# Kernel optimization log

Measured on AMD Instinct MI355X. Metric: run time of the kernel, lower is better.

## Reference

```python
import jax, jax.numpy as jnp
import numpy as np

B, S, D = 2, 2048, 2048
H, KVH, DH = 16, 4, 128  # n_heads, n_kv_heads, head_dim
N_REP = H // KVH
THETA = 10000.0


def setup_inputs() -> dict:
    key = jax.random.key(0)
    ks = jax.random.split(key, 6)
    x = jax.random.normal(ks[0], (B, S, D), dtype=jnp.float32)
    wq = jax.random.normal(ks[1], (H * DH, D), dtype=jnp.float32) * (D ** -0.5)
    wk = jax.random.normal(ks[2], (KVH * DH, D), dtype=jnp.float32) * (D ** -0.5)
    wv = jax.random.normal(ks[3], (KVH * DH, D), dtype=jnp.float32) * (D ** -0.5)
    wo = jax.random.normal(ks[4], (D, H * DH), dtype=jnp.float32) * (D ** -0.5)
    # RoPE frequencies (complex freqs -> cos/sin), shape [S, DH//2]
    inv_freq = 1.0 / (THETA ** (np.arange(0, DH, 2, dtype=np.float32) / DH))
    angles = np.arange(S, dtype=np.float32)[:, None] * inv_freq[None, :]
    freqs_cos = jnp.asarray(np.cos(angles))
    freqs_sin = jnp.asarray(np.sin(angles))
    # causal additive mask [1,1,S,S]
    neg = jnp.full((S, S), -1e9, dtype=jnp.float32)
    mask = jnp.triu(neg, k=1)[None, None]
    return {"x": x, "freqs_cos": freqs_cos, "freqs_sin": freqs_sin,
            "mask": mask, "wq": wq, "wk": wk, "wv": wv, "wo": wo}


def _rope(t, cos, sin):
    # t: [B,S,h,DH]; cos/sin: [S,DH//2] -> broadcast [1,S,1,DH//2]
    tp = t.reshape(*t.shape[:-1], -1, 2)
    tr, ti = tp[..., 0], tp[..., 1]
    c = cos[None, :, None, :]
    s = sin[None, :, None, :]
    out_r = tr * c - ti * s
    out_i = tr * s + ti * c
    return jnp.stack([out_r, out_i], axis=-1).reshape(t.shape)


def reference(x, freqs_cos, freqs_sin, mask, wq, wk, wv, wo):
    b, s, _ = x.shape
    xq = jnp.einsum('bsd,ed->bse', x, wq).reshape(b, s, H, DH)
    xk = jnp.einsum('bsd,ed->bse', x, wk).reshape(b, s, KVH, DH)
    xv = jnp.einsum('bsd,ed->bse', x, wv).reshape(b, s, KVH, DH)
    xq = _rope(xq, freqs_cos, freqs_sin)
    xk = _rope(xk, freqs_cos, freqs_sin)
    # GQA: repeat kv heads
    xk = jnp.repeat(xk, N_REP, axis=2)
    xv = jnp.repeat(xv, N_REP, axis=2)
    q = xq.transpose(0, 2, 1, 3)  # [B,H,S,DH]
    k = xk.transpose(0, 2, 1, 3)
    v = xv.transpose(0, 2, 1, 3)
    scores = jnp.einsum('bhqd,bhkd->bhqk', q, k) / jnp.sqrt(jnp.float32(DH))
    scores = scores + mask
    attn = jax.nn.softmax(scores.astype(jnp.float32), axis=-1).astype(q.dtype)
    out = jnp.einsum('bhqk,bhkd->bhqd', attn, v)
    out = out.transpose(0, 2, 1, 3).reshape(b, s, H * DH)
    return jnp.einsum('bse,de->bsd', out, wo)
```

## Files before the change

kernel.cpp:

```cpp
#include <hip/hip_runtime.h>

#define Bq   2
#define Sq   2048
#define Dq   2048
#define Hq   16
#define KVHq 4
#define DHq  128

typedef unsigned short u16;
typedef short  bf16x8 __attribute__((ext_vector_type(8)));
typedef float  f32x4  __attribute__((ext_vector_type(4)));
typedef float  f32x16 __attribute__((ext_vector_type(16)));
typedef unsigned short u16x2 __attribute__((ext_vector_type(2)));
typedef unsigned short u16x4 __attribute__((ext_vector_type(4)));
typedef unsigned uu32x4 __attribute__((ext_vector_type(4)));

__device__ __forceinline__ u16 f2bf(float f) {
    unsigned u = __float_as_uint(f);
    u += 0x7fffu + ((u >> 16) & 1u);
    return (u16)(u >> 16);
}
__device__ __forceinline__ float bf2f(u16 s) {
    return __uint_as_float(((unsigned)s) << 16);
}

__device__ __forceinline__ unsigned cvtpk(float a, float b) {
    unsigned r;
    asm("v_cvt_pk_bf16_f32 %0, %1, %2" : "=v"(r) : "v"(a), "v"(b));
    return r;
}
__device__ __forceinline__ void pl32swap(unsigned& a, unsigned& b) {
    asm("v_permlane32_swap_b32 %0, %1" : "+v"(a), "+v"(b));
}
__device__ __forceinline__ bf16x8 mkfrag(unsigned w0, unsigned w1, unsigned w2, unsigned w3) {
    uu32x4 t = {w0, w1, w2, w3};
    return __builtin_bit_cast(bf16x8, t);
}

__global__ void cast_all(const float* __restrict__ x,
                         const float* __restrict__ wq, const float* __restrict__ wk,
                         const float* __restrict__ wv, const float* __restrict__ wo,
                         u16* __restrict__ xb, u16* __restrict__ wqb,
                         u16* __restrict__ wkvb, u16* __restrict__ wob) {
    int i = blockIdx.x * 256 + threadIdx.x;
    const float4* src; u16x4* dst; int off;
    if (i < 2097152) { src = (const float4*)x; dst = (u16x4*)xb; off = i; }
    else {
        int j = i - 2097152;
        if (j < 1048576)      { src = (const float4*)wq; dst = (u16x4*)wqb;  off = j; }
        else if (j < 1310720) { src = (const float4*)wk; dst = (u16x4*)wkvb; off = j - 1048576; }
        else if (j < 1572864) { src = (const float4*)wv; dst = (u16x4*)wkvb + 262144; off = j - 1310720; }
        else                  { src = (const float4*)wo; dst = (u16x4*)wob;  off = j - 1572864; }
    }
    float4 v = src[off];
    u16x4 o;
    o.x = f2bf(v.x); o.y = f2bf(v.y); o.z = f2bf(v.z); o.w = f2bf(v.w);
    dst[off] = o;
}

__device__ __forceinline__ void async16(const void* g, void* l) {
    __builtin_amdgcn_global_load_lds(
        (const __attribute__((address_space(1))) unsigned*)g,
        (__attribute__((address_space(3))) unsigned*)l, 16, 0, 0);
}

__device__ __forceinline__ void stc(u16* p, float v)   { *p = f2bf(v); }
__device__ __forceinline__ void stc(float* p, float v) { *p = v; }

template <typename OutT>
__global__ __launch_bounds__(256) void gemm_nt(
    const u16* __restrict__ A, const u16* __restrict__ W, OutT* __restrict__ C,
    int M, int N, int K)
{
    __shared__ __align__(16) u16 lA[128 * 32];
    __shared__ __align__(16) u16 lB[128 * 32];

    const int t    = threadIdx.x;
    const int w    = t >> 6;
    const int lane = t & 63;
    const int lr   = lane & 15;
    const int quad = lane >> 4;
    const int wm   = (w >> 1) * 64, wn = (w & 1) * 64;
    const int bm   = blockIdx.x * 128, bn = blockIdx.y * 128;

    const u16* Ab = A + (size_t)bm * K;
    const u16* Wb = W + (size_t)bn * K;

    const int r0  = t >> 2;
    const int r1  = (256 + t) >> 2;
    const int kc0 = (t & 3) * 8;

    char* la0 = (char*)lA + w * 1024;
    char* la1 = (char*)lA + 4096 + w * 1024;
    char* lb0 = (char*)lB + w * 1024;
    char* lb1 = (char*)lB + 4096 + w * 1024;

    f32x4 acc[4][4] = {};

    for (int kt = 0; kt < K; kt += 32) {
        async16(Ab + (size_t)r0 * K + kt + kc0, la0);
        async16(Ab + (size_t)r1 * K + kt + kc0, la1);
        async16(Wb + (size_t)r0 * K + kt + kc0, lb0);
        async16(Wb + (size_t)r1 * K + kt + kc0, lb1);
        __syncthreads();

        bf16x8 af[4], bfr[4];
#pragma unroll
        for (int i = 0; i < 4; i++)
            af[i] = *(const bf16x8*)&lA[(wm + i * 16 + lr) * 32 + quad * 8];
#pragma unroll
        for (int j = 0; j < 4; j++)
            bfr[j] = *(const bf16x8*)&lB[(wn + j * 16 + lr) * 32 + quad * 8];
#pragma unroll
        for (int i = 0; i < 4; i++)
#pragma unroll
            for (int j = 0; j < 4; j++)
                acc[i][j] = __builtin_amdgcn_mfma_f32_16x16x32_bf16(af[i], bfr[j], acc[i][j], 0, 0, 0);
        __syncthreads();
    }

#pragma unroll
    for (int i = 0; i < 4; i++)
#pragma unroll
        for (int j = 0; j < 4; j++)
#pragma unroll
            for (int r = 0; r < 4; r++) {
                int gm = bm + wm + i * 16 + quad * 4 + r;
                int gn = bn + wn + j * 16 + lr;
                stc(C + (size_t)gm * N + gn, acc[i][j][r]);
            }
}

__global__ __launch_bounds__(256) void gemm_qkv(
    const u16* __restrict__ A, const u16* __restrict__ W,
    u16* __restrict__ Qo, u16* __restrict__ KVo,
    const float* __restrict__ Cs, const float* __restrict__ Sn)
{
    __shared__ __align__(16) u16 lA[128 * 32];
    __shared__ __align__(16) u16 lB[128 * 32];
    const int K = 2048;

    const int t    = threadIdx.x;
    const int w    = t >> 6;
    const int lane = t & 63;
    const int lr   = lane & 15;
    const int quad = lane >> 4;
    const int wm   = (w >> 1) * 64, wn = (w & 1) * 64;
    const int bm   = blockIdx.x * 128, bn = blockIdx.y * 128;

    const u16* Ab = A + (size_t)bm * K;
    const u16* Wb = W + (size_t)bn * K;

    const int r0  = t >> 2;
    const int r1  = (256 + t) >> 2;
    const int kc0 = (t & 3) * 8;

    char* la0 = (char*)lA + w * 1024;
    char* la1 = (char*)lA + 4096 + w * 1024;
    char* lb0 = (char*)lB + w * 1024;
    char* lb1 = (char*)lB + 4096 + w * 1024;

    f32x4 acc[4][4] = {};

    for (int kt = 0; kt < K; kt += 32) {
        async16(Ab + (size_t)r0 * K + kt + kc0, la0);
        async16(Ab + (size_t)r1 * K + kt + kc0, la1);
        async16(Wb + (size_t)r0 * K + kt + kc0, lb0);
        async16(Wb + (size_t)r1 * K + kt + kc0, lb1);
        __syncthreads();

        bf16x8 af[4], bfr[4];
#pragma unroll
        for (int i = 0; i < 4; i++)
            af[i] = *(const bf16x8*)&lA[(wm + i * 16 + lr) * 32 + quad * 8];
#pragma unroll
        for (int j = 0; j < 4; j++)
            bfr[j] = *(const bf16x8*)&lB[(wn + j * 16 + lr) * 32 + quad * 8];
#pragma unroll
        for (int i = 0; i < 4; i++)
#pragma unroll
            for (int j = 0; j < 4; j++)
                acc[i][j] = __builtin_amdgcn_mfma_f32_16x16x32_bf16(af[i], bfr[j], acc[i][j], 0, 0, 0);
        __syncthreads();
    }

    const bool doRope = (bn < 2560);
    const bool isQ    = (bn < 2048);
#pragma unroll
    for (int i = 0; i < 4; i++)
#pragma unroll
        for (int j = 0; j < 4; j++)
#pragma unroll
            for (int r = 0; r < 4; r++) {
                const int gm = bm + wm + i * 16 + quad * 4 + r;
                const int gn = bn + wn + j * 16 + lr;
                float v  = acc[i][j][r];
                float pv = __shfl_xor(v, 1);
                if (doRope) {
                    const int s = gm & (Sq - 1);
                    const int p = (gn & 127) >> 1;
                    const float cc = Cs[s * 64 + p], ss = Sn[s * 64 + p];
                    v = (gn & 1) ? (pv * ss + v * cc) : (v * cc - pv * ss);
                }
                const u16 ov = f2bf(v);
                if (isQ) Qo [(size_t)gm * 2048 + gn]          = ov;
                else     KVo[(size_t)gm * 1024 + (gn - 2048)] = ov;
            }
}

__global__ void transpose_v_k(const u16* __restrict__ KV, u16* __restrict__ Vt) {
    __shared__ u16 tile[32][33];
    const int bk = blockIdx.z;
    const int b = bk >> 2, kvh = bk & 3;
    const int s0 = blockIdx.x * 32, d0 = blockIdx.y * 32;
    const int tx = threadIdx.x, ty = threadIdx.y;
    tile[ty][tx] = KV[(size_t)(b * Sq + s0 + ty) * 1024 + 512 + kvh * 128 + d0 + tx];
    __syncthreads();
    Vt[((size_t)bk * DHq + d0 + ty) * Sq + s0 + tx] = tile[tx][ty];
}

#define PSCALE 0.12753102f
#define PBIAS  17.31234049f

__global__ __launch_bounds__(256, 2) void flash_attn_sk2(
    const u16* __restrict__ Q, const u16* __restrict__ KV,
    const u16* __restrict__ Vt, float* __restrict__ Oc, float* __restrict__ Lc)
{
    __shared__ __align__(16) u16 kl[2][4 * 64 * 32];
    __shared__ __align__(16) u16 vl[2][2 * 128 * 32];

    const int bh = blockIdx.x;
    const int b = bh >> 4, h = bh & 15;
    const int kvh = h >> 2;
    const int c = 39 - (int)blockIdx.y;
    int qt, ci, nc;
    if (c < 4)       { qt = c;                    ci = 0;            nc = 1; }
    else if (c < 12) { qt = 4  + ((c - 4) >> 1);  ci = (c - 4) & 1;  nc = 2; }
    else if (c < 24) { qt = 8  + (c - 12) / 3;    ci = (c - 12) % 3; nc = 3; }
    else             { qt = 12 + ((c - 24) >> 2); ci = (c - 24) & 3; nc = 4; }
    const int T  = 2 * (qt + 1);
    const int t0 = (ci * T) / nc, t1 = ((ci + 1) * T) / nc;

    const int tid = threadIdx.x;
    const int w = tid >> 6, lane = tid & 63;
    const int col = lane & 31, hi = lane >> 5;
    const int q0 = qt * 128 + w * 32;
    const int qg = q0 + col;

    const u16* Qp = Q + (size_t)(b * Sq + qg) * (Hq * DHq) + h * DHq + hi * 8;
    bf16x8 qf[8];
#pragma unroll
    for (int ks = 0; ks < 8; ks++) qf[ks] = *(const bf16x8*)(Qp + ks * 16);

    const u16* Kg = KV + (size_t)b * Sq * 1024 + kvh * DHq;
    const u16* Vg = Vt + (size_t)(b * KVHq + kvh) * DHq * Sq;

    const int srow = lane >> 2;
    const int swl  = ((lane & 3) ^ ((lane >> 3) & 3)) * 8;
    const int xsw  = (col >> 1) & 3;

    f32x16 o[4] = {};
    float lsum = 0.f;

    auto STAGE = [&](int kt, int bsel) {
        const int kb = kt * 64;
#pragma unroll
        for (int c4 = 0; c4 < 4; c4++) {
            const u16* g = Kg + (size_t)(kb + w * 16 + srow) * 1024 + c4 * 32 + swl;
            async16(g, (char*)kl[bsel] + (c4 * 2048 + w * 512) * 2 + lane * 16);
        }
#pragma unroll
        for (int c4 = 0; c4 < 4; c4++) {
            const int g2 = c4 & 1, dbase = (c4 >> 1) * 64;
            const u16* g = Vg + (size_t)(dbase + w * 16 + srow) * Sq + kb + g2 * 32 + swl;
            async16(g, (char*)vl[bsel] + (g2 * 4096 + (dbase + w * 16) * 32) * 2 + lane * 16);
        }
    };

    STAGE(t0, 0);
    __syncthreads();

    int cur = 0;
    for (int kt = t0; kt < t1; kt++) {
        if (kt + 1 < t1) STAGE(kt + 1, cur ^ 1);

        const int kb = kt * 64;
        const u16* klc = kl[cur];
        const u16* vlc = vl[cur];

        f32x16 s0 = {}, s1 = {};
        __builtin_amdgcn_s_setprio(1);
#pragma unroll
        for (int ks = 0; ks < 8; ks++) {
            const int ch     = (((ks & 1) * 2 + hi) ^ xsw) * 8;
            const int kkbase = (ks >> 1) * 2048 + ch;
            bf16x8 k0 = *(const bf16x8*)&klc[kkbase + col * 32];
            bf16x8 k1 = *(const bf16x8*)&klc[kkbase + (32 + col) * 32];
            s0 = __builtin_amdgcn_mfma_f32_32x32x16_bf16(k0, qf[ks], s0, 0, 0, 0);
            s1 = __builtin_amdgcn_mfma_f32_32x32x16_bf16(k1, qf[ks], s1, 0, 0, 0);
        }
        __builtin_amdgcn_s_setprio(0);

        float p0a[16], p1a[16];
        float ls = 0.f;
        if (q0 - kb >= 63) {
#pragma unroll
            for (int r = 0; r < 16; r++) {
                float a0 = exp2f(s0[r] * PSCALE - PBIAS);
                float a1 = exp2f(s1[r] * PSCALE - PBIAS);
                ls += a0 + a1;
                p0a[r] = a0; p1a[r] = a1;
            }
        } else {
            const int thr = qg - kb;
#pragma unroll
            for (int r = 0; r < 16; r++) {
                const int kloc = (r & 3) + 8 * (r >> 2) + 4 * hi;
                float a0 = (kloc <= thr)      ? exp2f(s0[r] * PSCALE - PBIAS) : 0.f;
                float a1 = (kloc + 32 <= thr) ? exp2f(s1[r] * PSCALE - PBIAS) : 0.f;
                ls += a0 + a1;
                p0a[r] = a0; p1a[r] = a1;
            }
        }
        lsum += ls;

        __builtin_amdgcn_s_setprio(1);
#define PV_HALF(PARR, KSBASE)                                                      \
        {                                                                          \
            _Pragma("unroll")                                                      \
            for (int k2 = 0; k2 < 2; k2++) {                                       \
                const int bb = k2 * 8;                                             \
                unsigned wa = cvtpk(PARR[bb + 0], PARR[bb + 1]);                   \
                unsigned wb = cvtpk(PARR[bb + 4], PARR[bb + 5]);                   \
                pl32swap(wa, wb);                                                  \
                unsigned wc = cvtpk(PARR[bb + 2], PARR[bb + 3]);                   \
                unsigned wd = cvtpk(PARR[bb + 6], PARR[bb + 7]);                   \
                pl32swap(wc, wd);                                                  \
                bf16x8 pa = mkfrag(wa, wc, wb, wd);                                \
                const int vch   = ((k2 * 2 + hi) ^ xsw) * 8;                       \
                const int vbase = (((KSBASE) >> 1) * 4096) + vch;                  \
                _Pragma("unroll")                                                  \
                for (int n = 0; n < 4; n++) {                                      \
                    bf16x8 vf = *(const bf16x8*)&vlc[vbase + (n * 32 + col) * 32]; \
                    o[n] = __builtin_amdgcn_mfma_f32_32x32x16_bf16(pa, vf, o[n], 0, 0, 0); \
                }                                                                  \
            }                                                                      \
        }
        PV_HALF(p0a, 0)
        PV_HALF(p1a, 2)
#undef PV_HALF
        __builtin_amdgcn_s_setprio(0);

        if (kt + 1 < t1) __syncthreads();
        cur ^= 1;
    }

    float tot = lsum + __shfl_xor(lsum, 32);
    float* Ocb = Oc + (size_t)(bh * 40 + c) * 16384 + (size_t)w * 32 * 128;
    float* Lcb = Lc + (size_t)(bh * 40 + c) * 128 + w * 32;
    if (hi == 0) Lcb[col] = tot;
#pragma unroll
    for (int r = 0; r < 16; r++) {
        const int rloc = (r & 3) + 8 * (r >> 2) + 4 * hi;
#pragma unroll
        for (int n = 0; n < 4; n++)
            Ocb[rloc * 128 + n * 32 + col] = o[n][r];
    }
}

__global__ __launch_bounds__(256) void flash_reduce2(
    const float* __restrict__ Oc, const float* __restrict__ Lc, u16* __restrict__ AO)
{
    const int bh = blockIdx.x;
    const int qt = blockIdx.y;
    const int e  = blockIdx.z * 256 + threadIdx.x;
    const int row = e >> 5, col4 = e & 31;
    int cst, nc;
    if (qt < 4)       { cst = qt;                 nc = 1; }
    else if (qt < 8)  { cst = 4  + 2 * (qt - 4);  nc = 2; }
    else if (qt < 12) { cst = 12 + 3 * (qt - 8);  nc = 3; }
    else              { cst = 24 + 4 * (qt - 12); nc = 4; }
    f32x4 acc = {0.f, 0.f, 0.f, 0.f};
    float l = 0.f;
    for (int i = 0; i < nc; i++) {
        const size_t base = (size_t)(bh * 40 + cst + i);
        acc += ((const f32x4*)(Oc + base * 16384))[e];
        l   += Lc[base * 128 + row];
    }
    const float inv = 1.0f / l;
    const int b = bh >> 4, h = bh & 15;
    u16x4 ov;
    ov.x = f2bf(acc[0] * inv); ov.y = f2bf(acc[1] * inv);
    ov.z = f2bf(acc[2] * inv); ov.w = f2bf(acc[3] * inv);
    u16* dst = AO + (size_t)(b * Sq + qt * 128 + row) * (Hq * DHq) + h * DHq + col4 * 4;
    *(u16x4*)dst = ov;
}

__global__ __launch_bounds__(256) void flash_attn(
    const u16* __restrict__ Q, const u16* __restrict__ KV,
    const u16* __restrict__ Vt, u16* __restrict__ O)
{
    __shared__ __align__(16) u16 plds[4][16 * 72];
    const int bh = blockIdx.x;
    const int b = bh >> 4, h = bh & 15;
    const int kvh = h >> 2;
    const int w = threadIdx.x >> 6, lane = threadIdx.x & 63;
    const int lr = lane & 15, quad = lane >> 4;
    const int yy = gridDim.y - 1 - blockIdx.y;
    const int q0 = yy * 64 + w * 16;

    const u16* Qp = Q + (size_t)(b * Sq + q0 + lr) * (Hq * DHq) + h * DHq + quad * 8;
    bf16x8 qf[4];
#pragma unroll
    for (int kk = 0; kk < 4; kk++) qf[kk] = *(const bf16x8*)(Qp + kk * 32);

    const u16* Kp = KV + (size_t)b * Sq * 1024 + kvh * DHq;
    const u16* Vp = Vt + (size_t)(b * KVHq + kvh) * DHq * Sq;

    f32x4 o[8] = {};
    float lsum[4] = {0.f, 0.f, 0.f, 0.f};

    const int nt = (q0 + 16 + 63) >> 6;
    for (int kt = 0; kt < nt; kt++) {
        const int kb = kt * 64;
        f32x4 s[4] = {};
#pragma unroll
        for (int kk = 0; kk < 4; kk++) {
#pragma unroll
            for (int j = 0; j < 4; j++) {
                bf16x8 kf = *(const bf16x8*)(Kp + (size_t)(kb + j * 16 + lr) * 1024 + kk * 32 + quad * 8);
                s[j] = __builtin_amdgcn_mfma_f32_16x16x32_bf16(qf[kk], kf, s[j], 0, 0, 0);
            }
        }
#pragma unroll
        for (int r = 0; r < 4; r++) {
            const int qg = q0 + quad * 4 + r;
#pragma unroll
            for (int j = 0; j < 4; j++) {
                float v = s[j][r] * PSCALE - PBIAS;
                float p = (kb + j * 16 + lr <= qg) ? exp2f(v) : 0.f;
                lsum[r] += p;
                plds[w][(quad * 4 + r) * 72 + j * 16 + lr] = f2bf(p);
            }
        }
        bf16x8 pa0 = *(const bf16x8*)&plds[w][lr * 72 + quad * 8];
        bf16x8 pa1 = *(const bf16x8*)&plds[w][lr * 72 + 32 + quad * 8];
#pragma unroll
        for (int dt = 0; dt < 8; dt++) {
            bf16x8 v0 = *(const bf16x8*)(Vp + (size_t)(dt * 16 + lr) * Sq + kb + quad * 8);
            bf16x8 v1 = *(const bf16x8*)(Vp + (size_t)(dt * 16 + lr) * Sq + kb + 32 + quad * 8);
            o[dt] = __builtin_amdgcn_mfma_f32_16x16x32_bf16(pa0, v0, o[dt], 0, 0, 0);
            o[dt] = __builtin_amdgcn_mfma_f32_16x16x32_bf16(pa1, v1, o[dt], 0, 0, 0);
        }
    }

    u16* Ob = O + (size_t)(b * Sq) * (Hq * DHq) + h * DHq;
#pragma unroll
    for (int r = 0; r < 4; r++) {
        float t = lsum[r];
        t += __shfl_xor(t, 1);
        t += __shfl_xor(t, 2);
        t += __shfl_xor(t, 4);
        t += __shfl_xor(t, 8);
        const float inv = 1.0f / t;
        const int qg = q0 + quad * 4 + r;
#pragma unroll
        for (int dt = 0; dt < 8; dt++)
            Ob[(size_t)qg * (Hq * DHq) + dt * 16 + lr] = f2bf(o[dt][r] * inv);
    }
}

extern "C" void kernel_launch(void* const* d_in, const int* in_sizes, int n_in,
                              void* d_out, int out_size, void* d_ws, size_t ws_size,
                              hipStream_t stream) {
    const float* x  = (const float*)d_in[0];
    const float* fc = (const float*)d_in[1];
    const float* fs = (const float*)d_in[2];
    const float* wq = (const float*)d_in[4];
    const float* wk = (const float*)d_in[5];
    const float* wv = (const float*)d_in[6];
    const float* wo = (const float*)d_in[7];
    float* out = (float*)d_out;

    char* ws = (char*)d_ws;
    u16* xb   = (u16*)(ws);
    u16* wqb  = (u16*)(ws + 16777216);
    u16* wkvb = (u16*)(ws + 25165824);
    u16* wob  = (u16*)(ws + 29360128);
    u16* Qb   = (u16*)(ws + 37748736);
    u16* KVb  = (u16*)(ws + 54525952);
    u16* Vtb  = (u16*)(ws + 62914560);
    u16* AOb  = (u16*)(ws + 67108864);
    float* Ocb = (float*)(ws + 83886080);
    float* Lcb = (float*)(ws + 167772160);
    const size_t WS_NEED = 168427520;

    cast_all<<<18432, 256, 0, stream>>>(x, wq, wk, wv, wo, xb, wqb, wkvb, wob);

    dim3 blk(256);
    gemm_qkv<<<dim3(32, 24), blk, 0, stream>>>(xb, wqb, Qb, KVb, fc, fs);

    transpose_v_k<<<dim3(64, 4, 8), dim3(32, 32), 0, stream>>>(KVb, Vtb);

    if (ws_size >= WS_NEED) {
        flash_attn_sk2<<<dim3(32, 40), blk, 0, stream>>>(Qb, KVb, Vtb, Ocb, Lcb);
        flash_reduce2<<<dim3(32, 16, 16), blk, 0, stream>>>(Ocb, Lcb, AOb);
    } else {
        flash_attn<<<dim3(32, 32), blk, 0, stream>>>(Qb, KVb, Vtb, AOb);
    }

    gemm_nt<float><<<dim3(32, 16), blk, 0, stream>>>(AOb, wob, out, 4096, 2048, 2048);
}
```

Before: 382.6 us.

## Double-buffer GEMM LDS tiles and XOR-swizzle columns to avoid bank conflicts

Both GEMM kernels now use two LDS buffers so the next K-tile's async global-to-LDS loads are issued before computing on the current tile, leaving one barrier per iteration. Column chunks are XOR-swizzled by row bits on load and unswizzled on read to reduce LDS bank conflicts on the bf16x8 fragment reads. This doubles LDS use per block, which may lower occupancy.

```diff
diff --git a/kernel.cpp b/kernel.cpp
--- a/kernel.cpp
+++ b/kernel.cpp
@@ -72,8 +72,8 @@
     const u16* __restrict__ A, const u16* __restrict__ W, OutT* __restrict__ C,
     int M, int N, int K)
 {
-    __shared__ __align__(16) u16 lA[128 * 32];
-    __shared__ __align__(16) u16 lB[128 * 32];
+    __shared__ __align__(16) u16 lA[2][128 * 32];
+    __shared__ __align__(16) u16 lB[2][128 * 32];
 
     const int t    = threadIdx.x;
     const int w    = t >> 6;
@@ -87,36 +87,40 @@
     const u16* Wb = W + (size_t)bn * K;
 
     const int r0  = t >> 2;
-    const int r1  = (256 + t) >> 2;
-    const int kc0 = (t & 3) * 8;
-
-    char* la0 = (char*)lA + w * 1024;
-    char* la1 = (char*)lA + 4096 + w * 1024;
-    char* lb0 = (char*)lB + w * 1024;
-    char* lb1 = (char*)lB + 4096 + w * 1024;
+    const int r1  = 64 + (t >> 2);
+    const int ksw = ((t & 3) ^ ((t >> 2) & 3) ^ ((t >> 4) & 3)) * 8;
+    const int cxr = (quad ^ (lr & 3) ^ (lr >> 2)) * 8;
 
     f32x4 acc[4][4] = {};
 
+    auto STAGE = [&](int kt, int bsel) {
+        async16(Ab + (size_t)r0 * K + kt + ksw, (char*)lA[bsel] + w * 1024);
+        async16(Ab + (size_t)r1 * K + kt + ksw, (char*)lA[bsel] + 4096 + w * 1024);
+        async16(Wb + (size_t)r0 * K + kt + ksw, (char*)lB[bsel] + w * 1024);
+        async16(Wb + (size_t)r1 * K + kt + ksw, (char*)lB[bsel] + 4096 + w * 1024);
+    };
+
+    STAGE(0, 0);
+    __syncthreads();
+
+    int cur = 0;
     for (int kt = 0; kt < K; kt += 32) {
-        async16(Ab + (size_t)r0 * K + kt + kc0, la0);
-        async16(Ab + (size_t)r1 * K + kt + kc0, la1);
-        async16(Wb + (size_t)r0 * K + kt + kc0, lb0);
-        async16(Wb + (size_t)r1 * K + kt + kc0, lb1);
-        __syncthreads();
+        if (kt + 32 < K) STAGE(kt + 32, cur ^ 1);
 
         bf16x8 af[4], bfr[4];
 #pragma unroll
         for (int i = 0; i < 4; i++)
-            af[i] = *(const bf16x8*)&lA[(wm + i * 16 + lr) * 32 + quad * 8];
+            af[i] = *(const bf16x8*)&lA[cur][(wm + i * 16 + lr) * 32 + cxr];
 #pragma unroll
         for (int j = 0; j < 4; j++)
-            bfr[j] = *(const bf16x8*)&lB[(wn + j * 16 + lr) * 32 + quad * 8];
+            bfr[j] = *(const bf16x8*)&lB[cur][(wn + j * 16 + lr) * 32 + cxr];
 #pragma unroll
         for (int i = 0; i < 4; i++)
 #pragma unroll
             for (int j = 0; j < 4; j++)
                 acc[i][j] = __builtin_amdgcn_mfma_f32_16x16x32_bf16(af[i], bfr[j], acc[i][j], 0, 0, 0);
         __syncthreads();
+        cur ^= 1;
     }
 
 #pragma unroll
@@ -136,8 +140,8 @@
     u16* __restrict__ Qo, u16* __restrict__ KVo,
     const float* __restrict__ Cs, const float* __restrict__ Sn)
 {
-    __shared__ __align__(16) u16 lA[128 * 32];
-    __shared__ __align__(16) u16 lB[128 * 32];
+    __shared__ __align__(16) u16 lA[2][128 * 32];
+    __shared__ __align__(16) u16 lB[2][128 * 32];
     const int K = 2048;
 
     const int t    = threadIdx.x;
@@ -152,36 +156,40 @@
     const u16* Wb = W + (size_t)bn * K;
 
     const int r0  = t >> 2;
-    const int r1  = (256 + t) >> 2;
-    const int kc0 = (t & 3) * 8;
-
-    char* la0 = (char*)lA + w * 1024;
-    char* la1 = (char*)lA + 4096 + w * 1024;
-    char* lb0 = (char*)lB + w * 1024;
-    char* lb1 = (char*)lB + 4096 + w * 1024;
+    const int r1  = 64 + (t >> 2);
+    const int ksw = ((t & 3) ^ ((t >> 2) & 3) ^ ((t >> 4) & 3)) * 8;
+    const int cxr = (quad ^ (lr & 3) ^ (lr >> 2)) * 8;
 
     f32x4 acc[4][4] = {};
 
+    auto STAGE = [&](int kt, int bsel) {
+        async16(Ab + (size_t)r0 * K + kt + ksw, (char*)lA[bsel] + w * 1024);
+        async16(Ab + (size_t)r1 * K + kt + ksw, (char*)lA[bsel] + 4096 + w * 1024);
+        async16(Wb + (size_t)r0 * K + kt + ksw, (char*)lB[bsel] + w * 1024);
+        async16(Wb + (size_t)r1 * K + kt + ksw, (char*)lB[bsel] + 4096 + w * 1024);
+    };
+
+    STAGE(0, 0);
+    __syncthreads();
+
+    int cur = 0;
     for (int kt = 0; kt < K; kt += 32) {
-        async16(Ab + (size_t)r0 * K + kt + kc0, la0);
-        async16(Ab + (size_t)r1 * K + kt + kc0, la1);
-        async16(Wb + (size_t)r0 * K + kt + kc0, lb0);
-        async16(Wb + (size_t)r1 * K + kt + kc0, lb1);
-        __syncthreads();
+        if (kt + 32 < K) STAGE(kt + 32, cur ^ 1);
 
         bf16x8 af[4], bfr[4];
 #pragma unroll
         for (int i = 0; i < 4; i++)
-            af[i] = *(const bf16x8*)&lA[(wm + i * 16 + lr) * 32 + quad * 8];
+            af[i] = *(const bf16x8*)&lA[cur][(wm + i * 16 + lr) * 32 + cxr];
 #pragma unroll
         for (int j = 0; j < 4; j++)
-            bfr[j] = *(const bf16x8*)&lB[(wn + j * 16 + lr) * 32 + quad * 8];
+            bfr[j] = *(const bf16x8*)&lB[cur][(wn + j * 16 + lr) * 32 + cxr];
 #pragma unroll
         for (int i = 0; i < 4; i++)
 #pragma unroll
             for (int j = 0; j < 4; j++)
                 acc[i][j] = __builtin_amdgcn_mfma_f32_16x16x32_bf16(af[i], bfr[j], acc[i][j], 0, 0, 0);
         __syncthreads();
+        cur ^= 1;
     }
 
     const bool doRope = (bn < 2560);
```

Measured after the change: 373.2 us. 2.5% less time.

## Double-buffer LDS tiles in GEMM kernels to overlap loads with MFMA

Applied to the files above, without the earlier changes.

Both the generic NT GEMM and the fused QKV+RoPE GEMM now keep two LDS buffers for A and W. The next K-slice is issued with async global-to-LDS loads before the MFMAs on the current slice run, and the loop is unrolled by two to alternate buffers. This is meant to hide global memory latency behind matrix-core work and to drop one barrier per K step. In exchange LDS use per block doubles, which can reduce occupancy. Correctness relies on the async loads being complete at the barrier, since there is no explicit vmcnt wait.

```diff
diff --git a/kernel.cpp b/kernel.cpp
--- a/kernel.cpp
+++ b/kernel.cpp
@@ -72,8 +72,8 @@
     const u16* __restrict__ A, const u16* __restrict__ W, OutT* __restrict__ C,
     int M, int N, int K)
 {
-    __shared__ __align__(16) u16 lA[128 * 32];
-    __shared__ __align__(16) u16 lB[128 * 32];
+    __shared__ __align__(16) u16 lA0[128 * 32], lA1[128 * 32];
+    __shared__ __align__(16) u16 lB0[128 * 32], lB1[128 * 32];
 
     const int t    = threadIdx.x;
     const int w    = t >> 6;
@@ -87,35 +87,41 @@
     const u16* Wb = W + (size_t)bn * K;
 
     const int r0  = t >> 2;
-    const int r1  = (256 + t) >> 2;
+    const int r1  = 64 + (t >> 2);
     const int kc0 = (t & 3) * 8;
 
-    char* la0 = (char*)lA + w * 1024;
-    char* la1 = (char*)lA + 4096 + w * 1024;
-    char* lb0 = (char*)lB + w * 1024;
-    char* lb1 = (char*)lB + 4096 + w * 1024;
-
     f32x4 acc[4][4] = {};
 
-    for (int kt = 0; kt < K; kt += 32) {
-        async16(Ab + (size_t)r0 * K + kt + kc0, la0);
-        async16(Ab + (size_t)r1 * K + kt + kc0, la1);
-        async16(Wb + (size_t)r0 * K + kt + kc0, lb0);
-        async16(Wb + (size_t)r1 * K + kt + kc0, lb1);
-        __syncthreads();
-
+    auto STAGE = [&](int kt, u16* la, u16* lb) {
+        async16(Ab + (size_t)r0 * K + kt + kc0, (char*)la + w * 1024);
+        async16(Ab + (size_t)r1 * K + kt + kc0, (char*)la + 4096 + w * 1024);
+        async16(Wb + (size_t)r0 * K + kt + kc0, (char*)lb + w * 1024);
+        async16(Wb + (size_t)r1 * K + kt + kc0, (char*)lb + 4096 + w * 1024);
+    };
+    auto COMPUTE = [&](const u16* la, const u16* lb) {
         bf16x8 af[4], bfr[4];
 #pragma unroll
         for (int i = 0; i < 4; i++)
-            af[i] = *(const bf16x8*)&lA[(wm + i * 16 + lr) * 32 + quad * 8];
+            af[i] = *(const bf16x8*)&la[(wm + i * 16 + lr) * 32 + quad * 8];
 #pragma unroll
         for (int j = 0; j < 4; j++)
-            bfr[j] = *(const bf16x8*)&lB[(wn + j * 16 + lr) * 32 + quad * 8];
+            bfr[j] = *(const bf16x8*)&lb[(wn + j * 16 + lr) * 32 + quad * 8];
 #pragma unroll
         for (int i = 0; i < 4; i++)
 #pragma unroll
             for (int j = 0; j < 4; j++)
                 acc[i][j] = __builtin_amdgcn_mfma_f32_16x16x32_bf16(af[i], bfr[j], acc[i][j], 0, 0, 0);
+    };
+
+    STAGE(0, lA0, lB0);
+    __syncthreads();
+
+    for (int kt = 0; kt < K; kt += 64) {
+        if (kt + 32 < K) STAGE(kt + 32, lA1, lB1);
+        COMPUTE(lA0, lB0);
+        __syncthreads();
+        if (kt + 64 < K) STAGE(kt + 64, lA0, lB0);
+        COMPUTE(lA1, lB1);
         __syncthreads();
     }
 
@@ -136,8 +142,8 @@
     u16* __restrict__ Qo, u16* __restrict__ KVo,
     const float* __restrict__ Cs, const float* __restrict__ Sn)
 {
-    __shared__ __align__(16) u16 lA[128 * 32];
-    __shared__ __align__(16) u16 lB[128 * 32];
+    __shared__ __align__(16) u16 lA0[128 * 32], lA1[128 * 32];
+    __shared__ __align__(16) u16 lB0[128 * 32], lB1[128 * 32];
     const int K = 2048;
 
     const int t    = threadIdx.x;
@@ -152,35 +158,41 @@
     const u16* Wb = W + (size_t)bn * K;
 
     const int r0  = t >> 2;
-    const int r1  = (256 + t) >> 2;
+    const int r1  = 64 + (t >> 2);
     const int kc0 = (t & 3) * 8;
 
-    char* la0 = (char*)lA + w * 1024;
-    char* la1 = (char*)lA + 4096 + w * 1024;
-    char* lb0 = (char*)lB + w * 1024;
-    char* lb1 = (char*)lB + 4096 + w * 1024;
-
     f32x4 acc[4][4] = {};
 
-    for (int kt = 0; kt < K; kt += 32) {
-        async16(Ab + (size_t)r0 * K + kt + kc0, la0);
-        async16(Ab + (size_t)r1 * K + kt + kc0, la1);
-        async16(Wb + (size_t)r0 * K + kt + kc0, lb0);
-        async16(Wb + (size_t)r1 * K + kt + kc0, lb1);
-        __syncthreads();
-
+    auto STAGE = [&](int kt, u16* la, u16* lb) {
+        async16(Ab + (size_t)r0 * K + kt + kc0, (char*)la + w * 1024);
+        async16(Ab + (size_t)r1 * K + kt + kc0, (char*)la + 4096 + w * 1024);
+        async16(Wb + (size_t)r0 * K + kt + kc0, (char*)lb + w * 1024);
+        async16(Wb + (size_t)r1 * K + kt + kc0, (char*)lb + 4096 + w * 1024);
+    };
+    auto COMPUTE = [&](const u16* la, const u16* lb) {
         bf16x8 af[4], bfr[4];
 #pragma unroll
         for (int i = 0; i < 4; i++)
-            af[i] = *(const bf16x8*)&lA[(wm + i * 16 + lr) * 32 + quad * 8];
+            af[i] = *(const bf16x8*)&la[(wm + i * 16 + lr) * 32 + quad * 8];
 #pragma unroll
         for (int j = 0; j < 4; j++)
-            bfr[j] = *(const bf16x8*)&lB[(wn + j * 16 + lr) * 32 + quad * 8];
+            bfr[j] = *(const bf16x8*)&lb[(wn + j * 16 + lr) * 32 + quad * 8];
 #pragma unroll
         for (int i = 0; i < 4; i++)
 #pragma unroll
             for (int j = 0; j < 4; j++)
                 acc[i][j] = __builtin_amdgcn_mfma_f32_16x16x32_bf16(af[i], bfr[j], acc[i][j], 0, 0, 0);
+    };
+
+    STAGE(0, lA0, lB0);
+    __syncthreads();
+
+    for (int kt = 0; kt < K; kt += 64) {
+        if (kt + 32 < K) STAGE(kt + 32, lA1, lB1);
+        COMPUTE(lA0, lB0);
+        __syncthreads();
+        if (kt + 64 < K) STAGE(kt + 64, lA0, lB0);
+        COMPUTE(lA1, lB1);
         __syncthreads();
     }
 
```

Result: faster. 358.3 us (-6.3%).

## Replace projection GEMMs with 256x256 double-buffered swizzled-LDS pipelined kernel

Applied to the files above, without the earlier changes.

Both the QKV projection (with fused RoPE epilogue) and the output projection move to a new 512-thread GEMM with 256x256 tiles, K-step 64, double-buffered LDS loaded asynchronously, XOR-swizzled LDS layout, and a hand-scheduled interleave of prefetch, LDS reads and MFMA quarters with priority bumps. The goal is to cut global/LDS traffic per FLOP and to overlap loads with matrix math, where the old kernel used small 128x128 tiles with a load-sync-compute loop. The trade-off is fewer blocks (192 and 128 workgroups), which may underfill the GPU's CUs, plus high register and LDS use.

```diff
diff --git a/kernel.cpp b/kernel.cpp
--- a/kernel.cpp
+++ b/kernel.cpp
@@ -64,148 +64,154 @@
         (__attribute__((address_space(3))) unsigned*)l, 16, 0, 0);
 }
 
-__device__ __forceinline__ void stc(u16* p, float v)   { *p = f2bf(v); }
-__device__ __forceinline__ void stc(float* p, float v) { *p = v; }
-
-template <typename OutT>
-__global__ __launch_bounds__(256) void gemm_nt(
+#define GBAR  __builtin_amdgcn_s_barrier()
+#define WAITL do { asm volatile("s_waitcnt lgkmcnt(0)" ::: "memory"); __builtin_amdgcn_sched_barrier(0); } while(0)
+#define WAITV4 asm volatile("s_waitcnt vmcnt(4)" ::: "memory")
+#define WAITV0 asm volatile("s_waitcnt vmcnt(0)" ::: "memory")
+#define SP1 __builtin_amdgcn_s_setprio(1)
+#define SP0 __builtin_amdgcn_s_setprio(0)
+
+#define LDA(BUF, MH) \
+    _Pragma("unroll") for (int ms = 0; ms < 4; ms++) \
+    _Pragma("unroll") for (int ks = 0; ks < 2; ks++) \
+        af[ms][ks] = *(const bf16x8*)&(BUF)[wm * 8192 + (((MH) * 64 + ms * 16 + lr) << 6) + (((ks * 4 + quad) ^ (lr & 7)) << 3)];
+
+#define LDB(BUF, NH) \
+    _Pragma("unroll") for (int ns = 0; ns < 2; ns++) \
+    _Pragma("unroll") for (int ks = 0; ks < 2; ks++) { \
+        const int n_ = wn * 64 + (NH) * 32 + ns * 16 + lr; \
+        bfr[NH][ns][ks] = *(const bf16x8*)&(BUF)[(n_ >> 7) * 8192 + ((n_ & 127) << 6) + (((ks * 4 + quad) ^ (lr & 7)) << 3)]; }
+
+#define MFMAQ(MH, NH) \
+    _Pragma("unroll") for (int ms = 0; ms < 4; ms++) \
+    _Pragma("unroll") for (int ns = 0; ns < 2; ns++) \
+    _Pragma("unroll") for (int ks = 0; ks < 2; ks++) \
+        acc[MH][NH][ms][ns] = __builtin_amdgcn_mfma_f32_16x16x32_bf16(af[ms][ks], bfr[NH][ns][ks], acc[MH][NH][ms][ns], 0, 0, 0);
+
+template <int EPI, typename OutT>
+__global__ __launch_bounds__(512, 2) void gemm256(
     const u16* __restrict__ A, const u16* __restrict__ W, OutT* __restrict__ C,
-    int M, int N, int K)
+    u16* __restrict__ Qo, u16* __restrict__ KVo,
+    const float* __restrict__ Cs, const float* __restrict__ Sn,
+    int N, int K)
 {
-    __shared__ __align__(16) u16 lA[128 * 32];
-    __shared__ __align__(16) u16 lB[128 * 32];
-
-    const int t    = threadIdx.x;
-    const int w    = t >> 6;
-    const int lane = t & 63;
+    __shared__ __align__(16) u16 lAb[2][16384];
+    __shared__ __align__(16) u16 lBb[2][16384];
+
+    const int tid  = threadIdx.x;
+    const int w    = tid >> 6, lane = tid & 63;
     const int lr   = lane & 15;
     const int quad = lane >> 4;
-    const int wm   = (w >> 1) * 64, wn = (w & 1) * 64;
-    const int bm   = blockIdx.x * 128, bn = blockIdx.y * 128;
-
-    const u16* Ab = A + (size_t)bm * K;
-    const u16* Wb = W + (size_t)bn * K;
-
-    const int r0  = t >> 2;
-    const int r1  = (256 + t) >> 2;
-    const int kc0 = (t & 3) * 8;
-
-    char* la0 = (char*)lA + w * 1024;
-    char* la1 = (char*)lA + 4096 + w * 1024;
-    char* lb0 = (char*)lB + w * 1024;
-    char* lb1 = (char*)lB + 4096 + w * 1024;
-
-    f32x4 acc[4][4] = {};
-
-    for (int kt = 0; kt < K; kt += 32) {
-        async16(Ab + (size_t)r0 * K + kt + kc0, la0);
-        async16(Ab + (size_t)r1 * K + kt + kc0, la1);
-        async16(Wb + (size_t)r0 * K + kt + kc0, lb0);
-        async16(Wb + (size_t)r1 * K + kt + kc0, lb1);
-        __syncthreads();
-
-        bf16x8 af[4], bfr[4];
-#pragma unroll
-        for (int i = 0; i < 4; i++)
-            af[i] = *(const bf16x8*)&lA[(wm + i * 16 + lr) * 32 + quad * 8];
-#pragma unroll
-        for (int j = 0; j < 4; j++)
-            bfr[j] = *(const bf16x8*)&lB[(wn + j * 16 + lr) * 32 + quad * 8];
-#pragma unroll
-        for (int i = 0; i < 4; i++)
-#pragma unroll
-            for (int j = 0; j < 4; j++)
-                acc[i][j] = __builtin_amdgcn_mfma_f32_16x16x32_bf16(af[i], bfr[j], acc[i][j], 0, 0, 0);
-        __syncthreads();
-    }
-
-#pragma unroll
-    for (int i = 0; i < 4; i++)
-#pragma unroll
-        for (int j = 0; j < 4; j++)
-#pragma unroll
-            for (int r = 0; r < 4; r++) {
-                int gm = bm + wm + i * 16 + quad * 4 + r;
-                int gn = bn + wn + j * 16 + lr;
-                stc(C + (size_t)gm * N + gn, acc[i][j][r]);
+    const int wm   = w >> 2, wn = w & 3;
+    const int bm   = blockIdx.x * 256, bn = blockIdx.y * 256;
+    const int NT   = K >> 6;
+
+    const u16* Ag = A + (size_t)bm * K;
+    const u16* Wg = W + (size_t)bn * K;
+    const size_t HK = (size_t)128 * K;
+
+    f32x4  acc[2][2][4][2] = {};
+    bf16x8 af[4][2];
+    bf16x8 bfr[2][2][2];
+
+    auto PF = [&](const u16* g, int kt, u16* dst) {
+#pragma unroll
+        for (int l = 0; l < 2; l++) {
+            const int cell = l * 512 + tid;
+            const int row  = cell >> 3;
+            const int ch   = (cell & 7) ^ (row & 7);
+            async16(g + (size_t)row * K + kt * 64 + ch * 8, (char*)dst + cell * 16);
+        }
+    };
+
+    PF(Wg,      0, lBb[0]);
+    PF(Wg + HK, 0, lBb[0] + 8192);
+    PF(Ag,      0, lAb[0]);
+    PF(Ag + HK, 0, lAb[0] + 8192);
+    PF(Wg,      1, lBb[1]);
+    PF(Wg + HK, 1, lBb[1] + 8192);
+    WAITV4;
+    GBAR;
+
+    for (int T = 0; T + 2 < NT; T += 2) {
+         LDA(lAb[0], 0); LDB(lBb[0], 0); PF(Ag,      T + 1, lAb[1]);
+               GBAR; WAITL; SP1; MFMAQ(0, 0); SP0; GBAR;
+         LDB(lBb[0], 1);                 PF(Ag + HK, T + 1, lAb[1] + 8192);
+               GBAR; WAITL; SP1; MFMAQ(0, 1); SP0; GBAR;
+         LDA(lAb[0], 1);                 PF(Wg,      T + 2, lBb[0]);
+               GBAR; WAITL; SP1; MFMAQ(1, 0); SP0; GBAR;
+                                         PF(Wg + HK, T + 2, lBb[0] + 8192);
+               GBAR; WAITL; SP1; MFMAQ(1, 1); SP0; WAITV4; GBAR;
+         LDA(lAb[1], 0); LDB(lBb[1], 0); PF(Ag,      T + 2, lAb[0]);
+               GBAR; WAITL; SP1; MFMAQ(0, 0); SP0; GBAR;
+         LDB(lBb[1], 1);                 PF(Ag + HK, T + 2, lAb[0] + 8192);
+               GBAR; WAITL; SP1; MFMAQ(0, 1); SP0; GBAR;
+         LDA(lAb[1], 1);                 PF(Wg,      T + 3, lBb[1]);
+               GBAR; WAITL; SP1; MFMAQ(1, 0); SP0; GBAR;
+                                         PF(Wg + HK, T + 3, lBb[1] + 8192);
+               GBAR; WAITL; SP1; MFMAQ(1, 1); SP0; WAITV4; GBAR;
+    }
+
+    {
+         LDA(lAb[0], 0); LDB(lBb[0], 0); PF(Ag,      NT - 1, lAb[1]);
+               GBAR; WAITL; SP1; MFMAQ(0, 0); SP0; GBAR;
+         LDB(lBb[0], 1);                 PF(Ag + HK, NT - 1, lAb[1] + 8192);
+               GBAR; WAITL; SP1; MFMAQ(0, 1); SP0; GBAR;
+         LDA(lAb[0], 1);
+               GBAR; WAITL; SP1; MFMAQ(1, 0); SP0; GBAR;
+         GBAR; SP1; MFMAQ(1, 1); SP0; WAITV0; GBAR;
+         LDA(lAb[1], 0); LDB(lBb[1], 0);
+               GBAR; WAITL; SP1; MFMAQ(0, 0); SP0; GBAR;
+         LDB(lBb[1], 1);
+               GBAR; WAITL; SP1; MFMAQ(0, 1); SP0; GBAR;
+         LDA(lAb[1], 1);
+               GBAR; WAITL; SP1; MFMAQ(1, 0); SP0; GBAR;
+         SP1; MFMAQ(1, 1); SP0;
+    }
+
+    if constexpr (EPI == 1) {
+        const bool doRope = (bn < 2560);
+        const bool isQ    = (bn < 2048);
+#pragma unroll
+        for (int mh = 0; mh < 2; mh++)
+#pragma unroll
+        for (int nh = 0; nh < 2; nh++)
+#pragma unroll
+        for (int ms = 0; ms < 4; ms++)
+#pragma unroll
+        for (int ns = 0; ns < 2; ns++)
+#pragma unroll
+        for (int r = 0; r < 4; r++) {
+            const int gm = bm + wm * 128 + mh * 64 + ms * 16 + quad * 4 + r;
+            const int gn = bn + wn * 64 + nh * 32 + ns * 16 + lr;
+            float v  = acc[mh][nh][ms][ns][r];
+            float pv = __shfl_xor(v, 1);
+            if (doRope) {
+                const int s = gm & (Sq - 1);
+                const int p = (gn & 127) >> 1;
+                const float cc = Cs[s * 64 + p], ss = Sn[s * 64 + p];
+                v = (gn & 1) ? (pv * ss + v * cc) : (v * cc - pv * ss);
             }
-}
-
-__global__ __launch_bounds__(256) void gemm_qkv(
-    const u16* __restrict__ A, const u16* __restrict__ W,
-    u16* __restrict__ Qo, u16* __restrict__ KVo,
-    const float* __restrict__ Cs, const float* __restrict__ Sn)
-{
-    __shared__ __align__(16) u16 lA[128 * 32];
-    __shared__ __align__(16) u16 lB[128 * 32];
-    const int K = 2048;
-
-    const int t    = threadIdx.x;
-    const int w    = t >> 6;
-    const int lane = t & 63;
-    const int lr   = lane & 15;
-    const int quad = lane >> 4;
-    const int wm   = (w >> 1) * 64, wn = (w & 1) * 64;
-    const int bm   = blockIdx.x * 128, bn = blockIdx.y * 128;
-
-    const u16* Ab = A + (size_t)bm * K;
-    const u16* Wb = W + (size_t)bn * K;
-
-    const int r0  = t >> 2;
-    const int r1  = (256 + t) >> 2;
-    const int kc0 = (t & 3) * 8;
-
-    char* la0 = (char*)lA + w * 1024;
-    char* la1 = (char*)lA + 4096 + w * 1024;
-    char* lb0 = (char*)lB + w * 1024;
-    char* lb1 = (char*)lB + 4096 + w * 1024;
-
-    f32x4 acc[4][4] = {};
-
-    for (int kt = 0; kt < K; kt += 32) {
-        async16(Ab + (size_t)r0 * K + kt + kc0, la0);
-        async16(Ab + (size_t)r1 * K + kt + kc0, la1);
-        async16(Wb + (size_t)r0 * K + kt + kc0, lb0);
-        async16(Wb + (size_t)r1 * K + kt + kc0, lb1);
-        __syncthreads();
-
-        bf16x8 af[4], bfr[4];
-#pragma unroll
-        for (int i = 0; i < 4; i++)
-            af[i] = *(const bf16x8*)&lA[(wm + i * 16 + lr) * 32 + quad * 8];
-#pragma unroll
-        for (int j = 0; j < 4; j++)
-            bfr[j] = *(const bf16x8*)&lB[(wn + j * 16 + lr) * 32 + quad * 8];
-#pragma unroll
-        for (int i = 0; i < 4; i++)
-#pragma unroll
-            for (int j = 0; j < 4; j++)
-                acc[i][j] = __builtin_amdgcn_mfma_f32_16x16x32_bf16(af[i], bfr[j], acc[i][j], 0, 0, 0);
-        __syncthreads();
-    }
-
-    const bool doRope = (bn < 2560);
-    const bool isQ    = (bn < 2048);
-#pragma unroll
-    for (int i = 0; i < 4; i++)
-#pragma unroll
-        for (int j = 0; j < 4; j++)
-#pragma unroll
-            for (int r = 0; r < 4; r++) {
-                const int gm = bm + wm + i * 16 + quad * 4 + r;
-                const int gn = bn + wn + j * 16 + lr;
-                float v  = acc[i][j][r];
-                float pv = __shfl_xor(v, 1);
-                if (doRope) {
-                    const int s = gm & (Sq - 1);
-                    const int p = (gn & 127) >> 1;
-                    const float cc = Cs[s * 64 + p], ss = Sn[s * 64 + p];
-                    v = (gn & 1) ? (pv * ss + v * cc) : (v * cc - pv * ss);
-                }
-                const u16 ov = f2bf(v);
-                if (isQ) Qo [(size_t)gm * 2048 + gn]          = ov;
-                else     KVo[(size_t)gm * 1024 + (gn - 2048)] = ov;
-            }
+            const u16 ov = f2bf(v);
+            if (isQ) Qo [(size_t)gm * 2048 + gn]          = ov;
+            else     KVo[(size_t)gm * 1024 + (gn - 2048)] = ov;
+        }
+    } else {
+#pragma unroll
+        for (int mh = 0; mh < 2; mh++)
+#pragma unroll
+        for (int nh = 0; nh < 2; nh++)
+#pragma unroll
+        for (int ms = 0; ms < 4; ms++)
+#pragma unroll
+        for (int ns = 0; ns < 2; ns++)
+#pragma unroll
+        for (int r = 0; r < 4; r++) {
+            const int gm = bm + wm * 128 + mh * 64 + ms * 16 + quad * 4 + r;
+            const int gn = bn + wn * 64 + nh * 32 + ns * 16 + lr;
+            C[(size_t)gm * N + gn] = acc[mh][nh][ms][ns][r];
+        }
+    }
 }
 
 __global__ void transpose_v_k(const u16* __restrict__ KV, u16* __restrict__ Vt) {
@@ -497,17 +503,19 @@
 
     cast_all<<<18432, 256, 0, stream>>>(x, wq, wk, wv, wo, xb, wqb, wkvb, wob);
 
-    dim3 blk(256);
-    gemm_qkv<<<dim3(32, 24), blk, 0, stream>>>(xb, wqb, Qb, KVb, fc, fs);
+    gemm256<1, float><<<dim3(16, 12), 512, 0, stream>>>(
+        xb, wqb, (float*)nullptr, Qb, KVb, fc, fs, 3072, 2048);
 
     transpose_v_k<<<dim3(64, 4, 8), dim3(32, 32), 0, stream>>>(KVb, Vtb);
 
     if (ws_size >= WS_NEED) {
-        flash_attn_sk2<<<dim3(32, 40), blk, 0, stream>>>(Qb, KVb, Vtb, Ocb, Lcb);
-        flash_reduce2<<<dim3(32, 16, 16), blk, 0, stream>>>(Ocb, Lcb, AOb);
+        flash_attn_sk2<<<dim3(32, 40), 256, 0, stream>>>(Qb, KVb, Vtb, Ocb, Lcb);
+        flash_reduce2<<<dim3(32, 16, 16), 256, 0, stream>>>(Ocb, Lcb, AOb);
     } else {
-        flash_attn<<<dim3(32, 32), blk, 0, stream>>>(Qb, KVb, Vtb, AOb);
-    }
-
-    gemm_nt<float><<<dim3(32, 16), blk, 0, stream>>>(AOb, wob, out, 4096, 2048, 2048);
-}
+        flash_attn<<<dim3(32, 32), 256, 0, stream>>>(Qb, KVb, Vtb, AOb);
+    }
+
+    gemm256<0, float><<<dim3(16, 8), 512, 0, stream>>>(
+        AOb, wob, out, (u16*)nullptr, (u16*)nullptr,
+        (const float*)nullptr, (const float*)nullptr, 2048, 2048);
+}
```

Result: no change. 381.5 us (-0.3%).
